# Kernel optimization log

Measured on AMD Instinct MI355X. Metric: run time of the kernel, lower is better.

The kernel has to match this reference:

```python
import jax, jax.numpy as jnp
import numpy as np

B, C, H, W = 8, 64, 64, 64
NPTS = 4096          # points per image
FX = 32              # extra per-point features
DOUT = 256
K = 3


def setup_inputs() -> dict:
    key = jax.random.key(0)
    k1, k2, k3, k4 = jax.random.split(key, 4)
    images = jax.random.normal(k1, (B, C, H, W), dtype=jnp.float32)
    x = jax.random.normal(k2, (B * NPTS, FX), dtype=jnp.float32)
    pos = jax.random.uniform(k3, (B * NPTS, 2), dtype=jnp.float32)
    batch = jnp.repeat(jnp.arange(B, dtype=jnp.int64), NPTS)
    W_nn = jax.random.normal(k4, (C + FX, DOUT), dtype=jnp.float32) / np.sqrt(C + FX)
    b_nn = jnp.zeros((DOUT,), dtype=jnp.float32)
    return {"images": images, "x": x, "pos": pos, "batch": batch,
            "W_nn": W_nn, "b_nn": b_nn, "k": K}


def reference(images, x, pos, batch, W_nn, b_nn, k):
    Bn, Cn, Hn, Wn = images.shape
    D = Hn
    P = D * D  # pixels per image
    # pixel features: [B, P, C]
    pix = jnp.transpose(images, (0, 2, 3, 1)).reshape(Bn, P, Cn)
    # pixel centers; flattened index i = r*D + c -> (centers[c], centers[r])
    centers = (jnp.arange(D, dtype=images.dtype) + 0.5) / D
    ppos = jnp.stack([jnp.tile(centers, D), jnp.repeat(centers, D)], axis=-1)  # [P, 2]
    # points are uniform per batch: [B, Npts, 2]
    pts = pos.reshape(Bn, -1, 2)
    # squared distances via |a|^2 + |b|^2 - 2 a.b -> [B, Npts, P]
    d2 = (jnp.sum(pts * pts, -1)[:, :, None]
          + jnp.sum(ppos * ppos, -1)[None, None, :]
          - 2.0 * jnp.einsum('bnd,pd->bnp', pts, ppos))
    neg_d2k, idx = jax.lax.top_k(-d2, k)            # k nearest pixels
    d2k = jnp.maximum(-neg_d2k, 1e-16)
    w = 1.0 / d2k                                    # [B, Npts, k]
    gathered = jax.vmap(lambda p, i: p[i])(pix, idx)  # [B, Npts, k, C]
    interp = jnp.sum(w[..., None] * gathered, axis=2) / jnp.sum(w, axis=2)[..., None]
    interp = interp.reshape(Bn * pts.shape[1], Cn)   # [N, C]
    h = jnp.concatenate([interp, x], axis=1)         # [N, C+FX]
    return h @ W_nn + b_nn                           # [N, DOUT]
```

## Files before the change

kernel.cpp:

```cpp
#include <hip/hip_runtime.h>
#include <hip/hip_bf16.h>

#define DD    64
#define PP    4096
#define NPTS  4096
#define NB    8
#define CCH   64
#define FXF   32
#define KIN   96
#define DOUT  256
#define NTOT  (NB*NPTS)

#define MTILE  64
#define HSTR   100
#define WCHUNK 16
#define NCHUNK (KIN / WCHUNK)

__global__ __launch_bounds__(256) void k_transpose(const float* __restrict__ img,
                                                   float* __restrict__ pix)
{
    __shared__ float tile[64][65];
    const int b  = blockIdx.z;
    const int p0 = blockIdx.x * 64;
    const int t  = threadIdx.x;

    const float* src = img + (size_t)b * CCH * PP;
    float*       dst = pix + (size_t)b * PP * CCH;

    {
        const int p4 = t & 15;
        const int ch = t >> 4;
#pragma unroll
        for (int i = 0; i < 64; i += 16) {
            const float4 v = ((const float4*)(src + (size_t)(ch + i) * PP + p0))[p4];
            *(float4*)&tile[ch + i][p4 * 4] = v;
        }
    }
    __syncthreads();
    {
        const int ch = t & 63;
        const int py = t >> 6;
#pragma unroll
        for (int i = 0; i < 64; i += 4)
            dst[(size_t)(p0 + py + i) * CCH + ch] = tile[ch][py + i];
    }
}

__global__ __launch_bounds__(512, 4) void k_fused(const float* __restrict__ pix,
                                                  const float* __restrict__ x,
                                                  const float* __restrict__ pos,
                                                  const float* __restrict__ Wn,
                                                  const float* __restrict__ bn,
                                                  float* __restrict__ out)
{
    __shared__ float h_lds[MTILE][HSTR];
    __shared__ float w_lds[WCHUNK * DOUT];

    const int t   = threadIdx.x;
    const int pt0 = blockIdx.x * MTILE;

    {
        const int lp  = t >> 3;
        const int q   = t & 7;
        const int gpt = pt0 + lp;
        const float2 pp = ((const float2*)pos)[gpt];
        const float px = pp.x;
        const float py = pp.y;
        const int   b  = gpt >> 12;

        const float spt = __fadd_rn(__fmul_rn(px, px), __fmul_rn(py, py));

        int cc = (int)floorf(px * 64.0f); cc = min(max(cc, 0), DD - 1);
        int rr = (int)floorf(py * 64.0f); rr = min(max(rr, 0), DD - 1);
        const int c0 = min(max(cc - 1, 0), DD - 3);
        const int r0 = min(max(rr - 1, 0), DD - 3);

        float bd0 = 1e30f, bd1 = 1e30f, bd2 = 1e30f;
        int   bp0 = 0,     bp1 = 0,     bp2 = 0;
#pragma unroll
        for (int dr = 0; dr < 3; ++dr) {
            const int   r  = r0 + dr;
            const float cy = ((float)r + 0.5f) * 0.015625f;
#pragma unroll
            for (int dc = 0; dc < 3; ++dc) {
                const int   c  = c0 + dc;
                const float cx = ((float)c + 0.5f) * 0.015625f;
                const float spp = __fadd_rn(__fmul_rn(cx, cx), __fmul_rn(cy, cy));
                const float dt  = __fmaf_rn(py, cy, __fmul_rn(px, cx));
                const float d2  = __fsub_rn(__fadd_rn(spt, spp), __fmul_rn(2.0f, dt));
                const int   p   = r * DD + c;
                if (d2 < bd2) {
                    if (d2 < bd1) {
                        if (d2 < bd0) { bd2 = bd1; bp2 = bp1; bd1 = bd0; bp1 = bp0; bd0 = d2; bp0 = p; }
                        else          { bd2 = bd1; bp2 = bp1; bd1 = d2;  bp1 = p; }
                    } else            { bd2 = d2;  bp2 = p; }
                }
            }
        }

        const float w0 = 1.0f / fmaxf(bd0, 1e-16f);
        const float w1 = 1.0f / fmaxf(bd1, 1e-16f);
        const float w2 = 1.0f / fmaxf(bd2, 1e-16f);
        const float inv = 1.0f / (w0 + w1 + w2);

        const float* g0p = pix + ((size_t)(b * PP + bp0)) * CCH + q * 8;
        const float* g1p = pix + ((size_t)(b * PP + bp1)) * CCH + q * 8;
        const float* g2p = pix + ((size_t)(b * PP + bp2)) * CCH + q * 8;
#pragma unroll
        for (int m = 0; m < 2; ++m) {
            const float4 g0 = ((const float4*)g0p)[m];
            const float4 g1 = ((const float4*)g1p)[m];
            const float4 g2 = ((const float4*)g2p)[m];
            float4 s;
            s.x = (w0 * g0.x + w1 * g1.x + w2 * g2.x) * inv;
            s.y = (w0 * g0.y + w1 * g1.y + w2 * g2.y) * inv;
            s.z = (w0 * g0.z + w1 * g1.z + w2 * g2.z) * inv;
            s.w = (w0 * g0.w + w1 * g1.w + w2 * g2.w) * inv;
            *(float4*)&h_lds[lp][q * 8 + m * 4] = s;
        }
        const float4 xv = *(const float4*)(x + (size_t)gpt * FXF + q * 4);
        *(float4*)&h_lds[lp][CCH + q * 4] = xv;
    }

    const int tx = t & 63;
    const int ty = t >> 6;

    float4 acc[8];
#pragma unroll
    for (int i = 0; i < 8; ++i) acc[i] = make_float4(0.f, 0.f, 0.f, 0.f);

    const float4 bias = *(const float4*)(bn + tx * 4);

    float4 wpre0 = ((const float4*)Wn)[t];
    float4 wpre1 = ((const float4*)Wn)[t + 512];

    for (int c = 0; c < NCHUNK; ++c) {
        __syncthreads();
        ((float4*)w_lds)[t]       = wpre0;
        ((float4*)w_lds)[t + 512] = wpre1;
        if (c + 1 < NCHUNK) {
            const float4* wsrc = (const float4*)(Wn + (size_t)(c + 1) * WCHUNK * DOUT);
            wpre0 = wsrc[t];
            wpre1 = wsrc[t + 512];
        }
        __syncthreads();

        const int k0 = c * WCHUNK;
#pragma unroll
        for (int kk = 0; kk < WCHUNK; kk += 4) {
            const float4 wv0 = *(const float4*)&w_lds[(kk + 0) * DOUT + tx * 4];
            const float4 wv1 = *(const float4*)&w_lds[(kk + 1) * DOUT + tx * 4];
            const float4 wv2 = *(const float4*)&w_lds[(kk + 2) * DOUT + tx * 4];
            const float4 wv3 = *(const float4*)&w_lds[(kk + 3) * DOUT + tx * 4];
#pragma unroll
            for (int i = 0; i < 8; ++i) {
                const float4 hv = *(const float4*)&h_lds[ty * 8 + i][k0 + kk];
                acc[i].x = fmaf(hv.x, wv0.x, fmaf(hv.y, wv1.x, fmaf(hv.z, wv2.x, fmaf(hv.w, wv3.x, acc[i].x))));
                acc[i].y = fmaf(hv.x, wv0.y, fmaf(hv.y, wv1.y, fmaf(hv.z, wv2.y, fmaf(hv.w, wv3.y, acc[i].y))));
                acc[i].z = fmaf(hv.x, wv0.z, fmaf(hv.y, wv1.z, fmaf(hv.z, wv2.z, fmaf(hv.w, wv3.z, acc[i].z))));
                acc[i].w = fmaf(hv.x, wv0.w, fmaf(hv.y, wv1.w, fmaf(hv.z, wv2.w, fmaf(hv.w, wv3.w, acc[i].w))));
            }
        }
    }

#pragma unroll
    for (int i = 0; i < 8; ++i) {
        float4 o;
        o.x = acc[i].x + bias.x; o.y = acc[i].y + bias.y;
        o.z = acc[i].z + bias.z; o.w = acc[i].w + bias.w;
        *(float4*)(out + ((size_t)(pt0 + ty * 8 + i)) * DOUT + tx * 4) = o;
    }
}

extern "C" void kernel_launch(void* const* d_in, const int* in_sizes, int n_in,
                              void* d_out, int out_size, void* d_ws, size_t ws_size,
                              hipStream_t stream)
{
    const float* images = (const float*)d_in[0];
    const float* x      = (const float*)d_in[1];
    const float* pos    = (const float*)d_in[2];
    const float* W_nn   = (const float*)d_in[4];
    const float* b_nn   = (const float*)d_in[5];
    float* out = (float*)d_out;

    float* pix = (float*)d_ws;

    k_transpose<<<dim3(PP / 64, 1, NB), 256, 0, stream>>>(images, pix);
    k_fused<<<NTOT / MTILE, 512, 0, stream>>>(pix, x, pos, W_nn, b_nn, out);
}
```

Measured before the change: 105.2 us.

## Use split-bf16 MFMA for projection GEMM with pre-swizzled weight fragments

Replaces the FP32 FMA GEMM with bf16 MFMA 16x16x32 instructions, using a hi/lo bf16 split (three MFMAs per tile) to keep close to fp32 accuracy. A new pre-kernel splits W into hi/lo bf16 halves laid out as MFMA B-fragments, so each wave loads them straight from global memory without an LDS staging loop. The block shrinks to 256 threads, and each wave owns 64 output columns. Output stores become scalar per-element writes instead of float4, and the extra launch plus the split arithmetic add overhead.

```diff
diff --git a/kernel.cpp b/kernel.cpp
--- a/kernel.cpp
+++ b/kernel.cpp
@@ -11,10 +11,26 @@
 #define DOUT  256
 #define NTOT  (NB*NPTS)
 
-#define MTILE  64
-#define HSTR   100
-#define WCHUNK 16
-#define NCHUNK (KIN / WCHUNK)
+#define MTILE 64
+#define KSTEPS 3
+#define NWAVES 4
+
+typedef float  f32x4  __attribute__((ext_vector_type(4)));
+typedef short  short8 __attribute__((ext_vector_type(8)));
+
+__device__ __forceinline__ void split_bf16(float v, unsigned short& hi, unsigned short& lo)
+{
+    union { float f; unsigned u; } a;
+    a.f = v;
+    unsigned r = (a.u + 0x7FFFu + ((a.u >> 16) & 1u)) >> 16;
+    hi = (unsigned short)r;
+    union { unsigned u; float f; } b;
+    b.u = r << 16;
+    float rem = v - b.f;
+    a.f = rem;
+    unsigned r2 = (a.u + 0x7FFFu + ((a.u >> 16) & 1u)) >> 16;
+    lo = (unsigned short)r2;
+}
 
 __global__ __launch_bounds__(256) void k_transpose(const float* __restrict__ img,
                                                    float* __restrict__ pix)
@@ -46,22 +62,48 @@
     }
 }
 
-__global__ __launch_bounds__(512, 4) void k_fused(const float* __restrict__ pix,
+__global__ __launch_bounds__(256) void k_wsplit(const float* __restrict__ Wn,
+                                                unsigned short* __restrict__ wfrag)
+{
+    const int t = blockIdx.x * 256 + threadIdx.x;
+    const int b  = t & 7;
+    const int l  = (t >> 3) & 63;
+    const int v  = t >> 9;
+    const int nr = v & 3;
+    const int w  = v >> 2;
+    const int ks = w % 3;
+    const int n  = w / 3;
+
+    const int k = ks * 32 + 8 * (l >> 4) + b;
+    const int d = n * 64 + nr * 16 + (l & 15);
+    const float val = Wn[k * DOUT + d];
+
+    unsigned short hi, lo;
+    split_bf16(val, hi, lo);
+    const int base = (((n * 3 + ks) * 2 + 0) * 4 + nr) * 512 + l * 8 + b;
+    const int basl = (((n * 3 + ks) * 2 + 1) * 4 + nr) * 512 + l * 8 + b;
+    wfrag[base] = hi;
+    wfrag[basl] = lo;
+}
+
+__global__ __launch_bounds__(256, 4) void k_fused(const float* __restrict__ pix,
                                                   const float* __restrict__ x,
                                                   const float* __restrict__ pos,
-                                                  const float* __restrict__ Wn,
+                                                  const unsigned short* __restrict__ wfrag,
                                                   const float* __restrict__ bn,
                                                   float* __restrict__ out)
 {
-    __shared__ float h_lds[MTILE][HSTR];
-    __shared__ float w_lds[WCHUNK * DOUT];
-
-    const int t   = threadIdx.x;
-    const int pt0 = blockIdx.x * MTILE;
+    __shared__ __align__(16) unsigned short h_hi[MTILE][KIN];
+    __shared__ __align__(16) unsigned short h_lo[MTILE][KIN];
+
+    const int t    = threadIdx.x;
+    const int lane = t & 63;
+    const int wv   = t >> 6;
+    const int pt0  = blockIdx.x * MTILE;
 
     {
-        const int lp  = t >> 3;
-        const int q   = t & 7;
+        const int lp  = t >> 2;
+        const int q   = t & 3;
         const int gpt = pt0 + lp;
         const float2 pp = ((const float2*)pos)[gpt];
         const float px = pp.x;
@@ -103,72 +145,97 @@
         const float w2 = 1.0f / fmaxf(bd2, 1e-16f);
         const float inv = 1.0f / (w0 + w1 + w2);
 
-        const float* g0p = pix + ((size_t)(b * PP + bp0)) * CCH + q * 8;
-        const float* g1p = pix + ((size_t)(b * PP + bp1)) * CCH + q * 8;
-        const float* g2p = pix + ((size_t)(b * PP + bp2)) * CCH + q * 8;
-#pragma unroll
-        for (int m = 0; m < 2; ++m) {
+        const float* g0p = pix + ((size_t)(b * PP + bp0)) * CCH + q * 16;
+        const float* g1p = pix + ((size_t)(b * PP + bp1)) * CCH + q * 16;
+        const float* g2p = pix + ((size_t)(b * PP + bp2)) * CCH + q * 16;
+#pragma unroll
+        for (int m = 0; m < 4; ++m) {
             const float4 g0 = ((const float4*)g0p)[m];
             const float4 g1 = ((const float4*)g1p)[m];
             const float4 g2 = ((const float4*)g2p)[m];
-            float4 s;
-            s.x = (w0 * g0.x + w1 * g1.x + w2 * g2.x) * inv;
-            s.y = (w0 * g0.y + w1 * g1.y + w2 * g2.y) * inv;
-            s.z = (w0 * g0.z + w1 * g1.z + w2 * g2.z) * inv;
-            s.w = (w0 * g0.w + w1 * g1.w + w2 * g2.w) * inv;
-            *(float4*)&h_lds[lp][q * 8 + m * 4] = s;
-        }
-        const float4 xv = *(const float4*)(x + (size_t)gpt * FXF + q * 4);
-        *(float4*)&h_lds[lp][CCH + q * 4] = xv;
-    }
-
-    const int tx = t & 63;
-    const int ty = t >> 6;
-
-    float4 acc[8];
-#pragma unroll
-    for (int i = 0; i < 8; ++i) acc[i] = make_float4(0.f, 0.f, 0.f, 0.f);
-
-    const float4 bias = *(const float4*)(bn + tx * 4);
-
-    float4 wpre0 = ((const float4*)Wn)[t];
-    float4 wpre1 = ((const float4*)Wn)[t + 512];
-
-    for (int c = 0; c < NCHUNK; ++c) {
-        __syncthreads();
-        ((float4*)w_lds)[t]       = wpre0;
-        ((float4*)w_lds)[t + 512] = wpre1;
-        if (c + 1 < NCHUNK) {
-            const float4* wsrc = (const float4*)(Wn + (size_t)(c + 1) * WCHUNK * DOUT);
-            wpre0 = wsrc[t];
-            wpre1 = wsrc[t + 512];
-        }
-        __syncthreads();
-
-        const int k0 = c * WCHUNK;
-#pragma unroll
-        for (int kk = 0; kk < WCHUNK; kk += 4) {
-            const float4 wv0 = *(const float4*)&w_lds[(kk + 0) * DOUT + tx * 4];
-            const float4 wv1 = *(const float4*)&w_lds[(kk + 1) * DOUT + tx * 4];
-            const float4 wv2 = *(const float4*)&w_lds[(kk + 2) * DOUT + tx * 4];
-            const float4 wv3 = *(const float4*)&w_lds[(kk + 3) * DOUT + tx * 4];
-#pragma unroll
-            for (int i = 0; i < 8; ++i) {
-                const float4 hv = *(const float4*)&h_lds[ty * 8 + i][k0 + kk];
-                acc[i].x = fmaf(hv.x, wv0.x, fmaf(hv.y, wv1.x, fmaf(hv.z, wv2.x, fmaf(hv.w, wv3.x, acc[i].x))));
-                acc[i].y = fmaf(hv.x, wv0.y, fmaf(hv.y, wv1.y, fmaf(hv.z, wv2.y, fmaf(hv.w, wv3.y, acc[i].y))));
-                acc[i].z = fmaf(hv.x, wv0.z, fmaf(hv.y, wv1.z, fmaf(hv.z, wv2.z, fmaf(hv.w, wv3.z, acc[i].z))));
-                acc[i].w = fmaf(hv.x, wv0.w, fmaf(hv.y, wv1.w, fmaf(hv.z, wv2.w, fmaf(hv.w, wv3.w, acc[i].w))));
+            float s[4];
+            s[0] = (w0 * g0.x + w1 * g1.x + w2 * g2.x) * inv;
+            s[1] = (w0 * g0.y + w1 * g1.y + w2 * g2.y) * inv;
+            s[2] = (w0 * g0.z + w1 * g1.z + w2 * g2.z) * inv;
+            s[3] = (w0 * g0.w + w1 * g1.w + w2 * g2.w) * inv;
+            ushort4 vh, vl;
+            split_bf16(s[0], vh.x, vl.x);
+            split_bf16(s[1], vh.y, vl.y);
+            split_bf16(s[2], vh.z, vl.z);
+            split_bf16(s[3], vh.w, vl.w);
+            *(ushort4*)&h_hi[lp][q * 16 + m * 4] = vh;
+            *(ushort4*)&h_lo[lp][q * 16 + m * 4] = vl;
+        }
+        const float4 xa = ((const float4*)(x + (size_t)gpt * FXF + q * 8))[0];
+        const float4 xb = ((const float4*)(x + (size_t)gpt * FXF + q * 8))[1];
+        ushort4 vh, vl;
+        split_bf16(xa.x, vh.x, vl.x);
+        split_bf16(xa.y, vh.y, vl.y);
+        split_bf16(xa.z, vh.z, vl.z);
+        split_bf16(xa.w, vh.w, vl.w);
+        *(ushort4*)&h_hi[lp][CCH + q * 8]     = vh;
+        *(ushort4*)&h_lo[lp][CCH + q * 8]     = vl;
+        split_bf16(xb.x, vh.x, vl.x);
+        split_bf16(xb.y, vh.y, vl.y);
+        split_bf16(xb.z, vh.z, vl.z);
+        split_bf16(xb.w, vh.w, vl.w);
+        *(ushort4*)&h_hi[lp][CCH + q * 8 + 4] = vh;
+        *(ushort4*)&h_lo[lp][CCH + q * 8 + 4] = vl;
+    }
+    __syncthreads();
+
+    f32x4 acc[4][4];
+#pragma unroll
+    for (int m = 0; m < 4; ++m)
+#pragma unroll
+        for (int n = 0; n < 4; ++n)
+            acc[m][n] = (f32x4)(0.0f);
+
+    const int arow = lane & 15;
+    const int aoct = (lane >> 4) * 8;
+
+    const unsigned short* wbase = wfrag + (size_t)wv * 3 * 2 * 4 * 512;
+
+#pragma unroll
+    for (int ks = 0; ks < KSTEPS; ++ks) {
+        const unsigned short* kb = wbase + ks * 2 * 4 * 512;
+        short8 Wh[4], Wl[4];
+#pragma unroll
+        for (int nr = 0; nr < 4; ++nr) {
+            Wh[nr] = *(const short8*)(kb + (0 * 4 + nr) * 512 + lane * 8);
+            Wl[nr] = *(const short8*)(kb + (1 * 4 + nr) * 512 + lane * 8);
+        }
+#pragma unroll
+        for (int m = 0; m < 4; ++m) {
+            const short8 Ah = *(const short8*)&h_hi[m * 16 + arow][ks * 32 + aoct];
+            const short8 Al = *(const short8*)&h_lo[m * 16 + arow][ks * 32 + aoct];
+#pragma unroll
+            for (int nr = 0; nr < 4; ++nr) {
+                acc[m][nr] = __builtin_amdgcn_mfma_f32_16x16x32_bf16(Ah, Wh[nr], acc[m][nr], 0, 0, 0);
+                acc[m][nr] = __builtin_amdgcn_mfma_f32_16x16x32_bf16(Al, Wh[nr], acc[m][nr], 0, 0, 0);
+                acc[m][nr] = __builtin_amdgcn_mfma_f32_16x16x32_bf16(Ah, Wl[nr], acc[m][nr], 0, 0, 0);
             }
         }
     }
 
-#pragma unroll
-    for (int i = 0; i < 8; ++i) {
-        float4 o;
-        o.x = acc[i].x + bias.x; o.y = acc[i].y + bias.y;
-        o.z = acc[i].z + bias.z; o.w = acc[i].w + bias.w;
-        *(float4*)(out + ((size_t)(pt0 + ty * 8 + i)) * DOUT + tx * 4) = o;
+    float bv[4];
+#pragma unroll
+    for (int nr = 0; nr < 4; ++nr)
+        bv[nr] = bn[wv * 64 + nr * 16 + (lane & 15)];
+
+    const int prow = (lane >> 4) * 4;
+    const int dcol = lane & 15;
+#pragma unroll
+    for (int m = 0; m < 4; ++m) {
+#pragma unroll
+        for (int nr = 0; nr < 4; ++nr) {
+#pragma unroll
+            for (int r = 0; r < 4; ++r) {
+                const int point = pt0 + m * 16 + prow + r;
+                const int dout  = wv * 64 + nr * 16 + dcol;
+                out[(size_t)point * DOUT + dout] = acc[m][nr][r] + bv[nr];
+            }
+        }
     }
 }
 
@@ -183,8 +250,10 @@
     const float* b_nn   = (const float*)d_in[5];
     float* out = (float*)d_out;
 
-    float* pix = (float*)d_ws;
-
+    float*          pix   = (float*)d_ws;
+    unsigned short* wfrag = (unsigned short*)((char*)d_ws + 8388608);
+
+    k_wsplit  <<<96, 256, 0, stream>>>(W_nn, wfrag);
     k_transpose<<<dim3(PP / 64, 1, NB), 256, 0, stream>>>(images, pix);
-    k_fused<<<NTOT / MTILE, 512, 0, stream>>>(pix, x, pos, W_nn, b_nn, out);
-}
+    k_fused   <<<NTOT / MTILE, 256, 0, stream>>>(pix, x, pos, wfrag, b_nn, out);
+}
```

New measurement: 96.05 us. 8.7% less time.
